# Kernel optimization log

Hardware: AMD Instinct MI355X
Metric: run time of the kernel (lower is better)

The kernel has to match this reference:

```python
import jax, jax.numpy as jnp
import numpy as np
import math

WIN = (24, 24)
NUM_HEADS = 16
RPB_DIM = 512
BS = 32
LOG2_8 = math.log2(8.0)  # 3.0


def _buffers():
    wh, ww = WIN
    # continuous log-scaled relative coordinate table: ((2wh-1)*(2ww-1), 2)
    rh = np.arange(-(wh - 1), wh, dtype=np.float32)
    rw = np.arange(-(ww - 1), ww, dtype=np.float32)
    table = np.stack(np.meshgrid(rh, rw, indexing='ij'), axis=-1)  # (2wh-1, 2ww-1, 2)
    table[..., 0] /= (wh - 1)
    table[..., 1] /= (ww - 1)
    table *= 8.0
    table = np.sign(table) * np.log2(np.abs(table) + 1.0) / LOG2_8
    coords_table = table.reshape(-1, 2).astype(np.float32)
    # relative position index: (N, N) with N = wh*ww
    ch = np.arange(wh)
    cw = np.arange(ww)
    coords = np.stack(np.meshgrid(ch, cw, indexing='ij'))  # (2, wh, ww)
    cf = coords.reshape(2, -1)                              # (2, N)
    rel = (cf[:, :, None] - cf[:, None, :]).transpose(1, 2, 0).copy()  # (N, N, 2)
    rel[:, :, 0] += wh - 1
    rel[:, :, 1] += ww - 1
    rel[:, :, 0] *= 2 * ww - 1
    rpi = rel.sum(-1).astype(np.int32)
    return coords_table, rpi


def setup_inputs() -> dict:
    key = jax.random.key(0)
    k1, k2, k3 = jax.random.split(key, 3)
    coords_table, rpi = _buffers()
    return {
        "glob_pos": jax.random.uniform(k1, (1, BS, 4), jnp.float32, 0.1, 1.0),
        "coords_table": jnp.asarray(coords_table),            # (T, 2)
        "rpi": jnp.asarray(rpi),                              # (N, N) int32
        "W1": jax.random.normal(k2, (2, RPB_DIM), jnp.float32) * 0.02,
        "b1": jnp.zeros((RPB_DIM,), jnp.float32),
        "W2": jax.random.normal(k3, (RPB_DIM, NUM_HEADS), jnp.float32) * 0.02,
        "num_prefix_tokens": 1,
    }


def reference(glob_pos, coords_table, rpi, W1, b1, W2, num_prefix_tokens):
    g = glob_pos[0]                       # squeeze(0) -> (bs, 4)
    pos_all = g[..., :2]                  # (bs, 2)
    pos = g[..., 2:]                      # (bs, 2)
    pos = (pos / pos_all) * 8.0
    pos = jnp.sign(pos) * jnp.log2(jnp.abs(pos) + 1.0) / LOG2_8
    pos = pos * 2.0 - 1.0
    # shifted coordinate table per sample: (bs, T, 2)
    table = coords_table[None, :, :] + pos[:, None, :]
    # tiny CPB MLP -> (bs, T, H)
    h = jax.nn.relu(jnp.einsum('btc,cd->btd', table, W1) + b1)
    bias = jnp.einsum('btd,dh->bth', h, W2)
    N = rpi.shape[0]
    bs = g.shape[0]
    H = W2.shape[1]
    P = num_prefix_tokens
    # gather per-pair bias: (bs, N, N, H)
    gathered = bias[:, rpi.reshape(-1)].reshape(bs, N, N, H)
    # zero-pad prefix rows/cols, then permute to (bs, H, N+P, N+P)
    result = jnp.zeros((bs, N + P, N + P, H), dtype=gathered.dtype)
    result = result.at[:, P:, P:].set(gathered)
    return jnp.transpose(result, (0, 3, 1, 2))
```

## Files before the change

### kernel.cpp

```cpp
#include <hip/hip_runtime.h>
#include <hip/hip_bf16.h>

#define TT    2209
#define NB    32
#define NH    16
#define ND    512
#define WH    24
#define NW    576
#define NP    577
#define PLANE (NP * NP)

__global__ __launch_bounds__(256) void cpb_mlp(
    const float* __restrict__ glob_pos,
    const float* __restrict__ coords_table,
    const float* __restrict__ W1,
    const float* __restrict__ b1,
    const float* __restrict__ W2,
    float* __restrict__ bias_t)
{
    const unsigned gid = blockIdx.x * 256u + threadIdx.x;
    const bool live = gid < (unsigned)(NB * TT);
    const unsigned b = live ? gid / TT : 0u;
    const unsigned t = live ? gid - b * TT : 0u;

    const float g0 = glob_pos[b * 4 + 0];
    const float g1 = glob_pos[b * 4 + 1];
    const float g2 = glob_pos[b * 4 + 2];
    const float g3 = glob_pos[b * 4 + 3];
    float px = g2 / g0 * 8.0f;
    float py = g3 / g1 * 8.0f;
    px = copysignf(log2f(fabsf(px) + 1.0f) * (1.0f / 3.0f), px) * 2.0f - 1.0f;
    py = copysignf(log2f(fabsf(py) + 1.0f) * (1.0f / 3.0f), py) * 2.0f - 1.0f;

    const float tx = coords_table[t * 2 + 0] + px;
    const float ty = coords_table[t * 2 + 1] + py;

    float acc[NH];
#pragma unroll
    for (int h = 0; h < NH; ++h) acc[h] = 0.0f;

#pragma unroll 2
    for (int d0 = 0; d0 < ND; d0 += 4) {
        const int du = __builtin_amdgcn_readfirstlane(d0);
        const float4 wa = *reinterpret_cast<const float4*>(W1 + du);
        const float4 wb = *reinterpret_cast<const float4*>(W1 + ND + du);
        const float4 bb = *reinterpret_cast<const float4*>(b1 + du);

        float hv[4];
        hv[0] = fmaxf(fmaf(tx, wa.x, fmaf(ty, wb.x, bb.x)), 0.0f);
        hv[1] = fmaxf(fmaf(tx, wa.y, fmaf(ty, wb.y, bb.y)), 0.0f);
        hv[2] = fmaxf(fmaf(tx, wa.z, fmaf(ty, wb.z, bb.z)), 0.0f);
        hv[3] = fmaxf(fmaf(tx, wa.w, fmaf(ty, wb.w, bb.w)), 0.0f);

#pragma unroll
        for (int k = 0; k < 4; ++k) {
            const float* w2row = W2 + (size_t)(du + k) * NH;
#pragma unroll
            for (int h = 0; h < NH; ++h) {
                acc[h] = fmaf(hv[k], w2row[h], acc[h]);
            }
        }
    }

    if (live) {
#pragma unroll
        for (int h = 0; h < NH; ++h) {
            bias_t[(b * NH + h) * TT + t] = acc[h];
        }
    }
}

__global__ __launch_bounds__(256) void cpb_scatter(
    const float* __restrict__ bias_t,
    float* __restrict__ out)
{
    constexpr unsigned TOTAL = (unsigned)NB * NH * PLANE;
    const unsigned gid  = blockIdx.x * 256u + threadIdx.x;
    const unsigned base = gid * 4u;
    if (base >= TOTAL) return;

    unsigned p   = base / PLANE;
    unsigned rem = base - p * PLANE;
    unsigned i   = rem / NP;
    unsigned j   = rem - i * NP;

    const float* __restrict__ plane = bias_t + (size_t)p * TT;

    float vals[4];
#pragma unroll
    for (int k = 0; k < 4; ++k) {
        float v = 0.0f;
        if (i != 0u && j != 0u) {
            const unsigned q  = i - 1u;
            const unsigned kk = j - 1u;
            const unsigned qh = q / WH,  qw = q - qh * WH;
            const unsigned kh = kk / WH, kw = kk - kh * WH;
            const unsigned idx = (qh - kh + (WH - 1u)) * (2u * WH - 1u)
                               + (qw - kw + (WH - 1u));
            v = plane[idx];
        }
        vals[k] = v;
        if (++j == (unsigned)NP) {
            j = 0u;
            if (++i == (unsigned)NP) { i = 0u; ++p; plane += TT; }
        }
    }

    float4 o;
    o.x = vals[0]; o.y = vals[1]; o.z = vals[2]; o.w = vals[3];
    *reinterpret_cast<float4*>(out + base) = o;
}

extern "C" void kernel_launch(void* const* d_in, const int* in_sizes, int n_in,
                              void* d_out, int out_size, void* d_ws, size_t ws_size,
                              hipStream_t stream)
{
    const float* glob_pos     = (const float*)d_in[0];
    const float* coords_table = (const float*)d_in[1];
    const float* W1           = (const float*)d_in[3];
    const float* b1           = (const float*)d_in[4];
    const float* W2           = (const float*)d_in[5];

    float* out    = (float*)d_out;
    float* bias_t = (float*)d_ws;

    const int n1 = NB * TT;
    const int blocks1 = (n1 + 255) / 256;
    cpb_mlp<<<blocks1, 256, 0, stream>>>(glob_pos, coords_table, W1, b1, W2, bias_t);

    const unsigned total   = (unsigned)NB * NH * PLANE;
    const unsigned groups  = total / 4u;
    const unsigned blocks2 = (groups + 255u) / 256u;
    cpb_scatter<<<blocks2, 256, 0, stream>>>(bias_t, out);
}
```

Measured before the change: 838.8 us.

## Stage MLP weights and per-plane bias tables in LDS, restructure scatter per plane

The MLP kernel now copies W1, b1 and W2 into shared memory once per block and reads them from LDS, replacing repeated global and scalar loads. The scatter kernel is reorganised so each block handles one chunk of a single (batch, head) plane. It loads that plane's 2209-entry bias table into LDS and gathers from there, with coalesced scalar stores. The catch is that float4 stores become scalar stores, and every block pays a preload and a barrier.

```diff
diff --git a/kernel.cpp b/kernel.cpp
--- a/kernel.cpp
+++ b/kernel.cpp
@@ -18,10 +18,28 @@
     const float* __restrict__ W2,
     float* __restrict__ bias_t)
 {
-    const unsigned gid = blockIdx.x * 256u + threadIdx.x;
-    const bool live = gid < (unsigned)(NB * TT);
-    const unsigned b = live ? gid / TT : 0u;
-    const unsigned t = live ? gid - b * TT : 0u;
+    __shared__ float sW13[ND][4];
+    __shared__ float sW2[ND][NH];
+
+    const int tid = threadIdx.x;
+    for (int d = tid; d < ND; d += 256) {
+        float4 v;
+        v.x = W1[d];
+        v.y = W1[ND + d];
+        v.z = b1[d];
+        v.w = 0.0f;
+        *reinterpret_cast<float4*>(&sW13[d][0]) = v;
+    }
+    for (int i = tid; i < ND * NH / 4; i += 256) {
+        reinterpret_cast<float4*>(&sW2[0][0])[i] =
+            reinterpret_cast<const float4*>(W2)[i];
+    }
+    __syncthreads();
+
+    const unsigned gid  = blockIdx.x * 256u + tid;
+    const bool     live = gid < (unsigned)(NB * TT);
+    const unsigned b    = live ? gid / TT : 0u;
+    const unsigned t    = live ? gid - b * TT : 0u;
 
     const float g0 = glob_pos[b * 4 + 0];
     const float g1 = glob_pos[b * 4 + 1];
@@ -39,26 +57,28 @@
 #pragma unroll
     for (int h = 0; h < NH; ++h) acc[h] = 0.0f;
 
-#pragma unroll 2
+#pragma unroll 1
     for (int d0 = 0; d0 < ND; d0 += 4) {
-        const int du = __builtin_amdgcn_readfirstlane(d0);
-        const float4 wa = *reinterpret_cast<const float4*>(W1 + du);
-        const float4 wb = *reinterpret_cast<const float4*>(W1 + ND + du);
-        const float4 bb = *reinterpret_cast<const float4*>(b1 + du);
-
         float hv[4];
-        hv[0] = fmaxf(fmaf(tx, wa.x, fmaf(ty, wb.x, bb.x)), 0.0f);
-        hv[1] = fmaxf(fmaf(tx, wa.y, fmaf(ty, wb.y, bb.y)), 0.0f);
-        hv[2] = fmaxf(fmaf(tx, wa.z, fmaf(ty, wb.z, bb.z)), 0.0f);
-        hv[3] = fmaxf(fmaf(tx, wa.w, fmaf(ty, wb.w, bb.w)), 0.0f);
-
 #pragma unroll
         for (int k = 0; k < 4; ++k) {
-            const float* w2row = W2 + (size_t)(du + k) * NH;
+            const float4 w = *reinterpret_cast<const float4*>(&sW13[d0 + k][0]);
+            hv[k] = fmaxf(fmaf(tx, w.x, fmaf(ty, w.y, w.z)), 0.0f);
+        }
 #pragma unroll
-            for (int h = 0; h < NH; ++h) {
-                acc[h] = fmaf(hv[k], w2row[h], acc[h]);
-            }
+        for (int k = 0; k < 4; ++k) {
+            const float4 w0 = *reinterpret_cast<const float4*>(&sW2[d0 + k][0]);
+            const float4 w1 = *reinterpret_cast<const float4*>(&sW2[d0 + k][4]);
+            const float4 w2 = *reinterpret_cast<const float4*>(&sW2[d0 + k][8]);
+            const float4 w3 = *reinterpret_cast<const float4*>(&sW2[d0 + k][12]);
+            acc[0]  = fmaf(hv[k], w0.x, acc[0]);   acc[1]  = fmaf(hv[k], w0.y, acc[1]);
+            acc[2]  = fmaf(hv[k], w0.z, acc[2]);   acc[3]  = fmaf(hv[k], w0.w, acc[3]);
+            acc[4]  = fmaf(hv[k], w1.x, acc[4]);   acc[5]  = fmaf(hv[k], w1.y, acc[5]);
+            acc[6]  = fmaf(hv[k], w1.z, acc[6]);   acc[7]  = fmaf(hv[k], w1.w, acc[7]);
+            acc[8]  = fmaf(hv[k], w2.x, acc[8]);   acc[9]  = fmaf(hv[k], w2.y, acc[9]);
+            acc[10] = fmaf(hv[k], w2.z, acc[10]);  acc[11] = fmaf(hv[k], w2.w, acc[11]);
+            acc[12] = fmaf(hv[k], w3.x, acc[12]);  acc[13] = fmaf(hv[k], w3.y, acc[13]);
+            acc[14] = fmaf(hv[k], w3.z, acc[14]);  acc[15] = fmaf(hv[k], w3.w, acc[15]);
         }
     }
 
@@ -70,45 +90,46 @@
     }
 }
 
+#define ELEMS 8
+#define CHUNK (256 * ELEMS)
+#define CPB   ((PLANE + CHUNK - 1) / CHUNK)
+
 __global__ __launch_bounds__(256) void cpb_scatter(
     const float* __restrict__ bias_t,
     float* __restrict__ out)
 {
-    constexpr unsigned TOTAL = (unsigned)NB * NH * PLANE;
-    const unsigned gid  = blockIdx.x * 256u + threadIdx.x;
-    const unsigned base = gid * 4u;
-    if (base >= TOTAL) return;
+    __shared__ float sPlane[TT];
 
-    unsigned p   = base / PLANE;
-    unsigned rem = base - p * PLANE;
-    unsigned i   = rem / NP;
-    unsigned j   = rem - i * NP;
+    const unsigned bx  = blockIdx.x;
+    const unsigned p   = bx / CPB;
+    const unsigned c   = bx - p * CPB;
+    const unsigned tid = threadIdx.x;
 
     const float* __restrict__ plane = bias_t + (size_t)p * TT;
+    for (unsigned idx = tid; idx < TT; idx += 256u) sPlane[idx] = plane[idx];
+    __syncthreads();
 
-    float vals[4];
+    const unsigned cb = c * CHUNK;
+    float* __restrict__ oplane = out + (size_t)p * PLANE;
+
 #pragma unroll
-    for (int k = 0; k < 4; ++k) {
-        float v = 0.0f;
-        if (i != 0u && j != 0u) {
-            const unsigned q  = i - 1u;
-            const unsigned kk = j - 1u;
-            const unsigned qh = q / WH,  qw = q - qh * WH;
-            const unsigned kh = kk / WH, kw = kk - kh * WH;
-            const unsigned idx = (qh - kh + (WH - 1u)) * (2u * WH - 1u)
-                               + (qw - kw + (WH - 1u));
-            v = plane[idx];
-        }
-        vals[k] = v;
-        if (++j == (unsigned)NP) {
-            j = 0u;
-            if (++i == (unsigned)NP) { i = 0u; ++p; plane += TT; }
+    for (int k = 0; k < ELEMS; ++k) {
+        const unsigned off = cb + tid + 256u * (unsigned)k;
+        if (off < (unsigned)PLANE) {
+            const unsigned i = off / NP;
+            const unsigned j = off - i * NP;
+            float v = 0.0f;
+            if (i != 0u && j != 0u) {
+                const unsigned q  = i - 1u;
+                const unsigned kk = j - 1u;
+                const unsigned qh = q / WH,  qw = q - qh * WH;
+                const unsigned kh = kk / WH, kw = kk - kh * WH;
+                v = sPlane[(qh - kh + (WH - 1u)) * (2u * WH - 1u)
+                           + (qw - kw + (WH - 1u))];
+            }
+            oplane[off] = v;
         }
     }
-
-    float4 o;
-    o.x = vals[0]; o.y = vals[1]; o.z = vals[2]; o.w = vals[3];
-    *reinterpret_cast<float4*>(out + base) = o;
 }
 
 extern "C" void kernel_launch(void* const* d_in, const int* in_sizes, int n_in,
@@ -128,8 +149,6 @@
     const int blocks1 = (n1 + 255) / 256;
     cpb_mlp<<<blocks1, 256, 0, stream>>>(glob_pos, coords_table, W1, b1, W2, bias_t);
 
-    const unsigned total   = (unsigned)NB * NH * PLANE;
-    const unsigned groups  = total / 4u;
-    const unsigned blocks2 = (groups + 255u) / 256u;
+    const unsigned blocks2 = (unsigned)NB * NH * CPB;
     cpb_scatter<<<blocks2, 256, 0, stream>>>(bias_t, out);
 }
```

New measurement: 886.4 us. 5.7% more time.
